# Kernel optimization log

Measured on AMD Instinct MI355X. Metric: run time of the kernel, lower is better.

The kernel has to match this reference:

```python
import jax, jax.numpy as jnp
import numpy as np

N = 50000
E = 800000
IN_C = 128
HID = 256
OUT_C = 51


def graph_conv(x, edge_index, edge_weight, w_rel, b_rel, w_root):
    # PyG GraphConv: out = lin_rel(aggr_add(w_e * x_src)) + lin_root(x)
    src, dst = edge_index[0], edge_index[1]
    msgs = x[src] * edge_weight[:, None]            # [E, F]
    agg = jax.ops.segment_sum(msgs, dst, num_segments=x.shape[0])  # [N, F]
    return agg @ w_rel + b_rel + x @ w_root


def setup_inputs() -> dict:
    key = jax.random.key(0)
    ks = jax.random.split(key, 10)
    s = lambda fan_in: 1.0 / np.sqrt(fan_in)
    return {
        "x0": jax.random.normal(ks[0], (N, IN_C), jnp.float32),
        "edge_index": jax.random.randint(ks[1], (2, E), 0, N, jnp.int64),
        "edge_weight": jax.random.uniform(ks[2], (E,), jnp.float32),
        "conv1_w_rel": jax.random.uniform(ks[3], (IN_C, HID), jnp.float32, -s(IN_C), s(IN_C)),
        "conv1_b_rel": jnp.zeros((HID,), jnp.float32),
        "conv1_w_root": jax.random.uniform(ks[4], (IN_C, HID), jnp.float32, -s(IN_C), s(IN_C)),
        "conv2_w_rel": jax.random.uniform(ks[5], (HID, HID), jnp.float32, -s(HID), s(HID)),
        "conv2_b_rel": jnp.zeros((HID,), jnp.float32),
        "conv2_w_root": jax.random.uniform(ks[6], (HID, HID), jnp.float32, -s(HID), s(HID)),
        "lin_w": jax.random.uniform(ks[7], (2 * HID, OUT_C), jnp.float32, -s(2 * HID), s(2 * HID)),
        "lin_b": jnp.zeros((OUT_C,), jnp.float32),
    }


def reference(x0, edge_index, edge_weight,
              conv1_w_rel, conv1_b_rel, conv1_w_root,
              conv2_w_rel, conv2_b_rel, conv2_w_root,
              lin_w, lin_b):
    # eval mode: dropout is identity
    x1 = jax.nn.relu(graph_conv(x0, edge_index, edge_weight, conv1_w_rel, conv1_b_rel, conv1_w_root))
    x2 = jax.nn.relu(graph_conv(x1, edge_index, edge_weight, conv2_w_rel, conv2_b_rel, conv2_w_root))
    x = jnp.concatenate([x1, x2], axis=-1)          # [N, 2H]
    return x @ lin_w + lin_b                         # [N, OUT_C]
```

## Files before the change

### kernel.cpp

```cpp
#include <hip/hip_runtime.h>
#include <hip/hip_bf16.h>

#define N_NODES 50000
#define N_EDGES 800000
#define IN_CH   128
#define HID     256
#define OUTC    51

typedef __attribute__((ext_vector_type(8))) short  bf16x8;
typedef __attribute__((ext_vector_type(4))) float  f32x4;
typedef __attribute__((ext_vector_type(2))) float  f32x2;
typedef __attribute__((ext_vector_type(4))) unsigned int u32x4;

__device__ __forceinline__ float bf2f(unsigned short u) {
    union { unsigned int i; float f; } v; v.i = ((unsigned int)u) << 16; return v.f;
}
__device__ __forceinline__ unsigned short f2bf(float f) {
    union { float f; unsigned int i; } v; v.f = f;
    unsigned int u = v.i;
    unsigned int r = (u + 0x7fffu + ((u >> 16) & 1u)) >> 16;
    return (unsigned short)r;
}
__device__ __forceinline__ unsigned short ldbf(const void* p, long i, int isf) {
    return isf ? f2bf(((const float*)p)[i]) : ((const unsigned short*)p)[i];
}
__device__ __forceinline__ float ldf(const void* p, long i, int isf) {
    return isf ? ((const float*)p)[i] : bf2f(((const unsigned short*)p)[i]);
}
__device__ __forceinline__ void load_edge_nt(const int* __restrict__ ei, int e, int is64,
                                             int* src, int* dst) {
    if (is64) { *src = __builtin_nontemporal_load(ei + 2 * e);
                *dst = __builtin_nontemporal_load(ei + 2 * (N_EDGES + e)); }
    else      { *src = __builtin_nontemporal_load(ei + e);
                *dst = __builtin_nontemporal_load(ei + N_EDGES + e); }
}

typedef const __attribute__((address_space(1))) unsigned int* gas_u32;
typedef __attribute__((address_space(3))) unsigned int* las_u32;
__device__ __forceinline__ void cp16(const void* g, void* l) {
    __builtin_amdgcn_global_load_lds((gas_u32)g, (las_u32)l, 16, 0, 0);
}

#define EBLK 1024
#define HB   ((N_EDGES + EBLK - 1) / EBLK)
#define NBKT ((N_NODES + 255) / 256)

#define NCHUNK ((N_NODES + 63) / 64)
#define ABLK   (NCHUNK * 4)

__global__ __launch_bounds__(256) void init_kernel(const unsigned int* __restrict__ x0w,
                                                   int* __restrict__ flags,
                                                   const int* __restrict__ ei) {
    int tid = threadIdx.x;
    if (blockIdx.x == 0) {
        if (tid < 64) {
            unsigned int w = x0w[tid];
            unsigned int ex = (w >> 7) & 0xFFu;
            unsigned long long bm = __ballot(ex >= 0x60u && ex <= 0x90u);
            if (tid == 0) flags[0] = (__popcll(bm) >= 48) ? 0 : 1;
        }
        return;
    }
    __shared__ int any;
    if (tid == 0) any = 0;
    __syncthreads();
    int acc = 0;
    for (int s = 0; s < 8; s++) {
        int i = (tid * 8 + s) * (N_EDGES / 2048);
        acc |= ei[2 * i + 1];
    }
    if (acc != 0) any = 1;
    __syncthreads();
    if (tid == 0) flags[1] = any;
}

__global__ void prep_all_kernel(const void* __restrict__ x0, int cb,
                                const void* __restrict__ w1r, const void* __restrict__ w1x,
                                const void* __restrict__ w2r, const void* __restrict__ w2x,
                                const void* __restrict__ lw,
                                const void* __restrict__ b1h, const void* __restrict__ b2h,
                                const void* __restrict__ lbh, const int* __restrict__ flags,
                                unsigned short* __restrict__ x0bf,
                                unsigned short* __restrict__ Bt1, unsigned short* __restrict__ Bt2,
                                unsigned short* __restrict__ Bt3,
                                float* __restrict__ b1, float* __restrict__ b2, float* __restrict__ b3,
                                const int* __restrict__ ei, unsigned int* __restrict__ bc,
                                int pblocks) {
    __shared__ unsigned int cnt[NBKT];
    int isf = flags[0];
    if ((int)blockIdx.x < cb) {
        if (!isf) return;
        long t0 = ((long)blockIdx.x * 256 + threadIdx.x) * 8;
        const float* xf = (const float*)x0;
        f32x4 v0 = *(const f32x4*)(xf + t0);
        f32x4 v1 = *(const f32x4*)(xf + t0 + 4);
        u32x4 pk;
        pk[0] = (unsigned int)f2bf(v0[0]) | ((unsigned int)f2bf(v0[1]) << 16);
        pk[1] = (unsigned int)f2bf(v0[2]) | ((unsigned int)f2bf(v0[3]) << 16);
        pk[2] = (unsigned int)f2bf(v1[0]) | ((unsigned int)f2bf(v1[1]) << 16);
        pk[3] = (unsigned int)f2bf(v1[2]) | ((unsigned int)f2bf(v1[3]) << 16);
        *(u32x4*)(x0bf + t0) = pk;
        return;
    }
    int rb = blockIdx.x - cb;
    if (rb >= pblocks) {
        int b = rb - pblocks;
        int tid = threadIdx.x;
        if (tid < NBKT) cnt[tid] = 0;
        __syncthreads();
        int is64 = (flags[1] == 0);
        int e0 = b * EBLK;
#pragma unroll
        for (int u = 0; u < 4; u++) {
            int e = e0 + u * 256 + tid;
            if (e < N_EDGES) {
                int src, dst; load_edge_nt(ei, e, is64, &src, &dst);
                if ((unsigned)src < N_NODES && (unsigned)dst < N_NODES)
                    atomicAdd(&cnt[dst >> 8], 1u);
            }
        }
        __syncthreads();
        if (tid < NBKT) bc[tid * HB + b] = cnt[tid];
        return;
    }
    int t = rb * 256 + threadIdx.x;
    if (t < 256 * 256) {
        int n = t >> 8, k = t & 255;
        Bt1[n * 256 + k] = (k < 128) ? ldbf(w1r, k * 256 + n, isf) : ldbf(w1x, (k - 128) * 256 + n, isf);
        return;
    }
    t -= 256 * 256;
    if (t < 256 * 512) {
        int n = t >> 9, k = t & 511;
        Bt2[n * 512 + k] = (k < 256) ? ldbf(w2r, k * 256 + n, isf) : ldbf(w2x, (k - 256) * 256 + n, isf);
        return;
    }
    t -= 256 * 512;
    if (t < 64 * 512) {
        int n = t >> 9, k = t & 511;
        Bt3[n * 512 + k] = (n < OUTC) ? ldbf(lw, k * OUTC + n, isf) : (unsigned short)0;
        return;
    }
    t -= 64 * 512;
    if (t < 256) { b1[t] = ldf(b1h, t, isf); return; }
    t -= 256;
    if (t < 256) { b2[t] = ldf(b2h, t, isf); return; }
    t -= 256;
    if (t < 64)  { b3[t] = (t < OUTC) ? ldf(lbh, t, isf) : 0.0f; return; }
}

__global__ __launch_bounds__(1024) void s1_kernel(const unsigned int* __restrict__ bc,
                                                  unsigned int* __restrict__ pbase,
                                                  unsigned int* __restrict__ total) {
    __shared__ unsigned int sd[1024];
    int b = blockIdx.x, tid = threadIdx.x;
    unsigned int v = (tid < HB) ? bc[b * HB + tid] : 0u;
    sd[tid] = v;
    __syncthreads();
    for (int off = 1; off < 1024; off <<= 1) {
        unsigned int t = (tid >= off) ? sd[tid - off] : 0u;
        __syncthreads();
        sd[tid] += t;
        __syncthreads();
    }
    if (tid < HB) pbase[tid * NBKT + b] = sd[tid] - v;
    if (tid == 1023) total[b] = sd[1023];
}

__global__ __launch_bounds__(256) void f1_kernel(const int* __restrict__ ei, const void* __restrict__ ew,
                                                 const int* __restrict__ flags,
                                                 const unsigned int* __restrict__ pbase,
                                                 const unsigned int* __restrict__ btot,
                                                 uint2* __restrict__ rec) {
    __shared__ unsigned int cur[NBKT];
    __shared__ unsigned int sb[256];
    int tid = threadIdx.x;
    unsigned int v = (tid < NBKT) ? btot[tid] : 0u;
    sb[tid] = v;
    __syncthreads();
    for (int off = 1; off < 256; off <<= 1) {
        unsigned int t = (tid >= off) ? sb[tid - off] : 0u;
        __syncthreads();
        sb[tid] += t;
        __syncthreads();
    }
    if (tid < NBKT) cur[tid] = (sb[tid] - v) + pbase[blockIdx.x * NBKT + tid];
    __syncthreads();
    int is64 = (flags[1] == 0);
    int isf = flags[0];
    int e0 = blockIdx.x * EBLK;
#pragma unroll
    for (int u = 0; u < 4; u++) {
        int e = e0 + u * 256 + tid;
        if (e < N_EDGES) {
            int src, dst; load_edge_nt(ei, e, is64, &src, &dst);
            if ((unsigned)src < N_NODES && (unsigned)dst < N_NODES) {
                unsigned int w = ldbf(ew, e, isf);
                unsigned int pos = atomicAdd(&cur[dst >> 8], 1u);
                uint2 r; r.x = (w << 16) | (unsigned)src; r.y = (unsigned)dst;
                rec[pos] = r;
            }
        }
    }
}

__global__ __launch_bounds__(512) void f2_kernel(const uint2* __restrict__ rec,
                                                 const unsigned int* __restrict__ btot,
                                                 int* __restrict__ rp, unsigned int* __restrict__ cw) {
    __shared__ unsigned int sb[256], c2[256], sc[256], cur2[256];
    int tid = threadIdx.x, b = blockIdx.x;
    unsigned int vb = 0;
    if (tid < 256) { vb = (tid < NBKT) ? btot[tid] : 0u; sb[tid] = vb; }
    __syncthreads();
    for (int off = 1; off < 256; off <<= 1) {
        unsigned int t = (tid < 256 && tid >= off) ? sb[tid - off] : 0u;
        __syncthreads();
        if (tid < 256) sb[tid] += t;
        __syncthreads();
    }
    unsigned int s0 = (b > 0) ? sb[b - 1] : 0u;
    unsigned int e0 = sb[b];
    if (b == 0 && tid == 0) rp[N_NODES] = (int)sb[NBKT - 1];
    if (tid < 256) c2[tid] = 0;
    __syncthreads();
    for (unsigned int pos = s0 + tid; pos < e0; pos += 512)
        atomicAdd(&c2[rec[pos].y & 255u], 1u);
    __syncthreads();
    unsigned int v = 0;
    if (tid < 256) { v = c2[tid]; sc[tid] = v; }
    __syncthreads();
    for (int off = 1; off < 256; off <<= 1) {
        unsigned int t = (tid < 256 && tid >= off) ? sc[tid - off] : 0u;
        __syncthreads();
        if (tid < 256) sc[tid] += t;
        __syncthreads();
    }
    if (tid < 256) {
        unsigned int start = s0 + sc[tid] - v;
        int node = b * 256 + tid;
        if (node < N_NODES) rp[node] = (int)start;
        cur2[tid] = start;
    }
    __syncthreads();
    for (unsigned int pos = s0 + tid; pos < e0; pos += 512) {
        uint2 r = rec[pos];
        unsigned int p = atomicAdd(&cur2[r.y & 255u], 1u);
        cw[p] = r.x;
    }
}

__global__ __launch_bounds__(256) void zout_kernel(unsigned short* __restrict__ out, long n) {
    long t = (long)blockIdx.x * 256 + threadIdx.x;
    if (t < n) out[t] = 0;
}

__global__ __launch_bounds__(256) void agg1_kernel(const unsigned short* __restrict__ x0raw,
                                                   const unsigned short* __restrict__ x0conv,
                                                   int use_conv, const int* __restrict__ flags,
                                                   const int* __restrict__ rp, const unsigned int* __restrict__ cw,
                                                   unsigned short* __restrict__ X12) {
    const unsigned short* x0b = (use_conv && flags[0]) ? x0conv : x0raw;
    int bid = blockIdx.x;
    int qq = (bid >> 1) & 3;
    int chunk = (bid >> 3) * 2 + (bid & 1);
    int g = threadIdx.x >> 4;
    int l = threadIdx.x & 15;
    int grpbase = threadIdx.x & 48;
    const unsigned short* tab = x0b + qq * 32 + l * 2;
#pragma unroll 1
    for (int i = 0; i < 4; i++) {
        int r = chunk * 64 + i * 16 + g;
        if (r >= N_NODES) continue;
        int js = rp[r], je = rp[r + 1];
        if (js < 0) js = 0;
        if (je > N_EDGES) je = N_EDGES;
        float a0 = 0.f, a1 = 0.f;
        for (int base = js; base < je; base += 16) {
            int n = je - base; if (n > 16) n = 16;
            int idx = base + l; if (idx >= je) idx = je - 1;
            unsigned int rec = __builtin_nontemporal_load(cw + idx);
            for (int j = 0; j < n; j += 8) {
                int m = n - j; if (m > 8) m = 8;
                unsigned int vv[8], qd[8];
#pragma unroll
                for (int u = 0; u < 8; u++) vv[u] = __shfl(rec, grpbase + j + u);
#pragma unroll
                for (int u = 0; u < 8; u++) if (u < m)
                    qd[u] = *(const unsigned int*)(tab + (long)(vv[u] & 0xFFFFu) * 128);
#pragma unroll
                for (int u = 0; u < 8; u++) if (u < m) {
                    float w = bf2f((unsigned short)(vv[u] >> 16));
                    a0 += w * bf2f((unsigned short)(qd[u] & 0xffffu));
                    a1 += w * bf2f((unsigned short)(qd[u] >> 16));
                }
            }
        }
        *(unsigned int*)&X12[(long)r * 512 + 256 + qq * 32 + l * 2] =
            (unsigned int)f2bf(a0) | ((unsigned int)f2bf(a1) << 16);
    }
}

__global__ __launch_bounds__(256) void agg2_kernel(const int* __restrict__ rp, const unsigned int* __restrict__ cw,
                                                   unsigned short* __restrict__ X12,
                                                   const unsigned char* __restrict__ x1f8,
                                                   const int* __restrict__ flags, int f8mode) {
    int usef8 = (f8mode == 2) || (f8mode == 1 && flags[0] == 0);
    int bid = blockIdx.x;
    int qq = (bid >> 1) & 3;
    int chunk = (bid >> 3) * 2 + (bid & 1);
    int g = threadIdx.x >> 4;
    int l = threadIdx.x & 15;
    int grpbase = threadIdx.x & 48;
#pragma unroll 1
    for (int i = 0; i < 4; i++) {
        int r = chunk * 64 + i * 16 + g;
        if (r >= N_NODES) continue;
        int js = rp[r], je = rp[r + 1];
        if (js < 0) js = 0;
        if (je > N_EDGES) je = N_EDGES;
        float a0 = 0.f, a1 = 0.f, a2 = 0.f, a3 = 0.f;
        if (usef8) {
            const unsigned char* tab = x1f8 + qq * 64 + l * 4;
            for (int base = js; base < je; base += 16) {
                int n = je - base; if (n > 16) n = 16;
                int idx = base + l; if (idx >= je) idx = je - 1;
                unsigned int rec = __builtin_nontemporal_load(cw + idx);
                for (int j = 0; j < n; j += 8) {
                    int m = n - j; if (m > 8) m = 8;
                    unsigned int vv[8], qd[8];
#pragma unroll
                    for (int u = 0; u < 8; u++) vv[u] = __shfl(rec, grpbase + j + u);
#pragma unroll
                    for (int u = 0; u < 8; u++) if (u < m)
                        qd[u] = *(const unsigned int*)(tab + (long)(vv[u] & 0xFFFFu) * 256);
#pragma unroll
                    for (int u = 0; u < 8; u++) if (u < m) {
                        float w = bf2f((unsigned short)(vv[u] >> 16));
                        f32x2 plo = __builtin_amdgcn_cvt_pk_f32_fp8((int)qd[u], false);
                        f32x2 phi = __builtin_amdgcn_cvt_pk_f32_fp8((int)qd[u], true);
                        a0 += w * plo.x; a1 += w * plo.y;
                        a2 += w * phi.x; a3 += w * phi.y;
                    }
                }
            }
        } else {
            const unsigned short* tabb = X12 + qq * 64 + l * 4;
            for (int base = js; base < je; base += 16) {
                int n = je - base; if (n > 16) n = 16;
                int idx = base + l; if (idx >= je) idx = je - 1;
                unsigned int rec = __builtin_nontemporal_load(cw + idx);
                for (int j = 0; j < n; j += 8) {
                    int m = n - j; if (m > 8) m = 8;
                    unsigned int vv[8]; uint2 qd[8];
#pragma unroll
                    for (int u = 0; u < 8; u++) vv[u] = __shfl(rec, grpbase + j + u);
#pragma unroll
                    for (int u = 0; u < 8; u++) if (u < m)
                        qd[u] = *(const uint2*)(tabb + (long)(vv[u] & 0xFFFFu) * 512);
#pragma unroll
                    for (int u = 0; u < 8; u++) if (u < m) {
                        float w = bf2f((unsigned short)(vv[u] >> 16));
                        a0 += w * bf2f((unsigned short)(qd[u].x & 0xffffu));
                        a1 += w * bf2f((unsigned short)(qd[u].x >> 16));
                        a2 += w * bf2f((unsigned short)(qd[u].y & 0xffffu));
                        a3 += w * bf2f((unsigned short)(qd[u].y >> 16));
                    }
                }
            }
        }
        uint2 pk;
        pk.x = (unsigned int)f2bf(a0) | ((unsigned int)f2bf(a1) << 16);
        pk.y = (unsigned int)f2bf(a2) | ((unsigned int)f2bf(a3) << 16);
        *(uint2*)&X12[(long)r * 512 + 256 + qq * 64 + l * 4] = pk;
    }
}

__global__ __launch_bounds__(512) void gemm_big_kernel(
    const unsigned short* __restrict__ Aagg, int lda_agg, int Kagg,
    const unsigned short* __restrict__ AxRaw, const unsigned short* __restrict__ AxConv,
    int use_conv, int lda_x,
    const unsigned short* __restrict__ Bt, int K,
    const float* __restrict__ bias, const int* __restrict__ flags,
    unsigned short* __restrict__ out, int ldo, int ocol, int M,
    unsigned char* __restrict__ x1f8, int f8mode) {
    __shared__ __align__(16) unsigned short As[128][64];
    __shared__ __align__(16) unsigned short Bs[256][64];
    const unsigned short* Ax = (use_conv && flags[0]) ? AxConv : AxRaw;
    int dof8 = (f8mode == 2) || (f8mode == 1 && flags[0] == 0);
    int tid = threadIdx.x;
    int bm0 = blockIdx.x * 128;
    int wave = tid >> 6, lane = tid & 63;
    int wm = wave >> 2, wn = wave & 3;
    int quad = lane >> 4, l16 = lane & 15;
    int lr = lane >> 3;
    int sc = (lane & 7) ^ lr;

    f32x4 acc[4][4];
#pragma unroll
    for (int mt = 0; mt < 4; mt++)
#pragma unroll
        for (int nt = 0; nt < 4; nt++) acc[mt][nt] = (f32x4){0.f, 0.f, 0.f, 0.f};

    for (int k0 = 0; k0 < K; k0 += 64) {
        const unsigned short* srcp;
        int stride, koff;
        if (k0 < Kagg) { srcp = Aagg; stride = lda_agg; koff = k0; }
        else           { srcp = Ax;   stride = lda_x;   koff = k0 - Kagg; }
#pragma unroll
        for (int i = 0; i < 2; i++) {
            int t = wave * 2 + i;
            int r = t * 8 + lr;
            int gr = bm0 + r; if (gr >= M) gr = M - 1;
            cp16(srcp + (long)gr * stride + koff + sc * 8, (char*)As + t * 1024);
        }
#pragma unroll
        for (int i = 0; i < 4; i++) {
            int t = wave * 4 + i;
            int r = t * 8 + lr;
            cp16(Bt + (long)r * K + k0 + sc * 8, (char*)Bs + t * 1024);
        }
        __syncthreads();
#pragma unroll
        for (int kc = 0; kc < 64; kc += 32) {
            int k8 = (kc >> 3) + quad;
            int swz = (k8 ^ (l16 & 7)) << 4;
            bf16x8 a[4], b[4];
#pragma unroll
            for (int mt = 0; mt < 4; mt++) {
                int row = wm * 64 + mt * 16 + l16;
                a[mt] = *(const bf16x8*)((const char*)As + row * 128 + swz);
            }
#pragma unroll
            for (int nt = 0; nt < 4; nt++) {
                int row = wn * 64 + nt * 16 + l16;
                b[nt] = *(const bf16x8*)((const char*)Bs + row * 128 + swz);
            }
#pragma unroll
            for (int mt = 0; mt < 4; mt++)
#pragma unroll
                for (int nt = 0; nt < 4; nt++)
                    acc[mt][nt] = __builtin_amdgcn_mfma_f32_16x16x32_bf16(a[mt], b[nt], acc[mt][nt], 0, 0, 0);
        }
        __syncthreads();
    }

#pragma unroll
    for (int mt = 0; mt < 4; mt++) {
#pragma unroll
        for (int nt = 0; nt < 4; nt++) {
            f32x4 a = acc[mt][nt];
            int colI = wn * 64 + nt * 16 + l16;
            float bv = bias[colI];
#pragma unroll
            for (int rr = 0; rr < 4; rr++) {
                int row = bm0 + wm * 64 + mt * 16 + quad * 4 + rr;
                if (row < M) {
                    float v = a[rr] + bv;
                    v = v > 0.f ? v : 0.f;
                    out[(long)row * ldo + ocol + colI] = f2bf(v);
                    if (dof8) {
                        int p = __builtin_amdgcn_cvt_pk_fp8_f32(v, v, 0, false);
                        x1f8[(long)row * 256 + colI] = (unsigned char)(p & 0xff);
                    }
                }
            }
        }
    }
}

__global__ __launch_bounds__(256) void gemm_head_kernel(
    const unsigned short* __restrict__ Ax, int lda_x,
    const unsigned short* __restrict__ Bt, int K,
    const float* __restrict__ bias,
    void* __restrict__ out, int ldo,
    int M, int realN, const int* __restrict__ flagF) {
    __shared__ __align__(16) unsigned short As[64][64];
    __shared__ __align__(16) unsigned short Bs[64][64];
    int tid = threadIdx.x;
    int bm0 = blockIdx.x * 64;
    int wave = tid >> 6, lane = tid & 63;
    int wm = wave >> 1, wn = wave & 1;
    int quad = lane >> 4, l16 = lane & 15;
    int lr = lane >> 3;
    int sc = (lane & 7) ^ lr;

    f32x4 acc[2][2];
#pragma unroll
    for (int mt = 0; mt < 2; mt++)
#pragma unroll
        for (int nt = 0; nt < 2; nt++) acc[mt][nt] = (f32x4){0.f, 0.f, 0.f, 0.f};

    for (int k0 = 0; k0 < K; k0 += 64) {
#pragma unroll
        for (int i = 0; i < 2; i++) {
            int t = wave * 2 + i;
            int r = t * 8 + lr;
            int gr = bm0 + r; if (gr >= M) gr = M - 1;
            cp16(Ax + (long)gr * lda_x + k0 + sc * 8, (char*)As + t * 1024);
        }
#pragma unroll
        for (int i = 0; i < 2; i++) {
            int t = wave * 2 + i;
            int r = t * 8 + lr;
            cp16(Bt + (long)r * K + k0 + sc * 8, (char*)Bs + t * 1024);
        }
        __syncthreads();
#pragma unroll
        for (int kc = 0; kc < 64; kc += 32) {
            int k8 = (kc >> 3) + quad;
            int swz = (k8 ^ (l16 & 7)) << 4;
            bf16x8 a0 = *(const bf16x8*)((const char*)As + (wm * 32 + l16) * 128 + swz);
            bf16x8 a1 = *(const bf16x8*)((const char*)As + (wm * 32 + 16 + l16) * 128 + swz);
#pragma unroll
            for (int nt = 0; nt < 2; nt++) {
                bf16x8 b = *(const bf16x8*)((const char*)Bs + (wn * 32 + nt * 16 + l16) * 128 + swz);
                acc[0][nt] = __builtin_amdgcn_mfma_f32_16x16x32_bf16(a0, b, acc[0][nt], 0, 0, 0);
                acc[1][nt] = __builtin_amdgcn_mfma_f32_16x16x32_bf16(a1, b, acc[1][nt], 0, 0, 0);
            }
        }
        __syncthreads();
    }

    int out_f32 = *flagF;
#pragma unroll
    for (int mt = 0; mt < 2; mt++) {
#pragma unroll
        for (int nt = 0; nt < 2; nt++) {
            f32x4 a = acc[mt][nt];
            int colI = wn * 32 + nt * 16 + l16;
            float bv = bias[colI];
#pragma unroll
            for (int rr = 0; rr < 4; rr++) {
                int row = bm0 + wm * 32 + mt * 16 + quad * 4 + rr;
                if (row < M && colI < realN) {
                    float v = a[rr] + bv;
                    long idx = (long)row * ldo + colI;
                    if (out_f32) ((float*)out)[idx] = v;
                    else ((unsigned short*)out)[idx] = f2bf(v);
                }
            }
        }
    }
}

extern "C" void kernel_launch(void* const* d_in, const int* in_sizes, int n_in,
                              void* d_out, int out_size, void* d_ws, size_t ws_size,
                              hipStream_t stream) {
    const void* x0  = d_in[0];
    const int*  ei  = (const int*)d_in[1];
    const void* ew  = d_in[2];
    const void* w1r = d_in[3];
    const void* b1h = d_in[4];
    const void* w1x = d_in[5];
    const void* w2r = d_in[6];
    const void* b2h = d_in[7];
    const void* w2x = d_in[8];
    const void* lw  = d_in[9];
    const void* lbh = d_in[10];

    char* ws = (char*)d_ws;
    unsigned short* X12     = (unsigned short*)(ws);
    unsigned int*   cw      = (unsigned int*)(ws + 51200000);
    int*            row_ptr = (int*)(ws + 54400000);
    unsigned short* Bt1     = (unsigned short*)(ws + 54800128);
    unsigned short* Bt2     = (unsigned short*)(ws + 54931200);
    unsigned short* Bt3     = (unsigned short*)(ws + 55193344);
    float*          b1      = (float*)(ws + 55258880);
    float*          b2      = (float*)(ws + 55259904);
    float*          b3      = (float*)(ws + 55260928);
    int*            flags   = (int*)(ws + 55261184);
    unsigned short* x0bf    = (unsigned short*)(ws + 55262272);
    unsigned char*  x1f8sep = (unsigned char*)(ws + 68062272);
    const size_t NEED_NOCONV = 55262272;
    const size_t NEED_FULL   = 68062272;
    const size_t NEED_F8SEP  = 80862272;

    uint2*        rec   = (uint2*)(ws);
    unsigned int* bc    = (unsigned int*)(ws + 6400000);
    unsigned int* pbse  = (unsigned int*)(ws + 7013120);
    unsigned int* btot  = (unsigned int*)(ws + 7626240);

    if (ws_size < NEED_NOCONV) {
        long n = (long)N_NODES * OUTC;
        zout_kernel<<<(int)((n + 255) / 256), 256, 0, stream>>>((unsigned short*)d_out, n);
        return;
    }
    int use_conv = (ws_size >= NEED_FULL) ? 1 : 0;
    int f8mode = (ws_size >= NEED_F8SEP) ? 2 : (use_conv ? 1 : 0);
    unsigned char* x1f8 = (f8mode == 2) ? x1f8sep : (unsigned char*)x0bf;

    int* flagF = flags + 0;

    init_kernel<<<2, 256, 0, stream>>>((const unsigned int*)x0, flags, ei);

    int cb = use_conv ? ((N_NODES * IN_CH) / (256 * 8)) : 0;
    {
        int ptotal = 256 * 256 + 256 * 512 + 64 * 512 + 256 + 256 + 64;
        int pblocks = (ptotal + 255) / 256;
        prep_all_kernel<<<cb + pblocks + HB, 256, 0, stream>>>(
            x0, cb, w1r, w1x, w2r, w2x, lw, b1h, b2h, lbh, flags, x0bf,
            Bt1, Bt2, Bt3, b1, b2, b3, ei, bc, pblocks);
    }

    s1_kernel<<<NBKT, 1024, 0, stream>>>(bc, pbse, btot);
    f1_kernel<<<HB, 256, 0, stream>>>(ei, ew, flags, pbse, btot, rec);
    f2_kernel<<<NBKT, 512, 0, stream>>>(rec, btot, row_ptr, cw);

    int mblocks  = (N_NODES + 127) / 128;
    int hblocks  = (N_NODES + 63) / 64;

    const unsigned short* x0raw = (const unsigned short*)x0;

    agg1_kernel<<<ABLK, 256, 0, stream>>>(x0raw, x0bf, use_conv, flags, row_ptr, cw, X12);
    gemm_big_kernel<<<mblocks, 512, 0, stream>>>(X12 + 256, 512, 128,
                                                 x0raw, x0bf, use_conv, IN_CH,
                                                 Bt1, 256, b1, flags,
                                                 X12, 512, 0, N_NODES, x1f8, f8mode);
    agg2_kernel<<<ABLK, 256, 0, stream>>>(row_ptr, cw, X12, x1f8, flags, f8mode);
    gemm_big_kernel<<<mblocks, 512, 0, stream>>>(X12 + 256, 512, 256,
                                                 X12, X12, 0, 512,
                                                 Bt2, 512, b2, flags,
                                                 X12, 512, 256, N_NODES, (unsigned char*)nullptr, 0);
    gemm_head_kernel<<<hblocks, 256, 0, stream>>>(X12, 512, Bt3, 512, b3,
                                                  d_out, OUTC, N_NODES, OUTC, flagF);
}
```

Measured before the change: 294.9 us.

## Gather full rows in agg1 and split fp8 x1 table into column quarters

agg1 now assigns one 16-lane group per destination row and gathers each source's full 128-feature row with 16-byte loads, replacing four passes over the edge list with 4-byte loads. The fp8 copy of x1 is stored as four 64-column planes (QSZ apart), so each agg2 quarter gathers from a compact 3.2 MB table that is more likely to stay cache-resident. Trade-offs are higher register use for eight accumulators in agg1 and an fp8 buffer layout that must hold 4*QSZ bytes.

```diff
diff --git a/kernel.cpp b/kernel.cpp
--- a/kernel.cpp
+++ b/kernel.cpp
@@ -6,6 +6,8 @@
 #define IN_CH   128
 #define HID     256
 #define OUTC    51
+
+#define QSZ 3200000
 
 typedef __attribute__((ext_vector_type(8))) short  bf16x8;
 typedef __attribute__((ext_vector_type(4))) float  f32x4;
@@ -46,7 +48,7 @@
 #define NBKT ((N_NODES + 255) / 256)
 
 #define NCHUNK ((N_NODES + 63) / 64)
-#define ABLK   (NCHUNK * 4)
+#define ABLKQ  (NCHUNK * 4)
 
 __global__ __launch_bounds__(256) void init_kernel(const unsigned int* __restrict__ x0w,
                                                    int* __restrict__ flags,
@@ -260,57 +262,62 @@
                                                    const int* __restrict__ rp, const unsigned int* __restrict__ cw,
                                                    unsigned short* __restrict__ X12) {
     const unsigned short* x0b = (use_conv && flags[0]) ? x0conv : x0raw;
+    int r = blockIdx.x * 16 + (threadIdx.x >> 4);
+    if (r >= N_NODES) return;
+    int l = threadIdx.x & 15;
+    int grpbase = threadIdx.x & 48;
+    int js = rp[r], je = rp[r + 1];
+    if (js < 0) js = 0;
+    if (je > N_EDGES) je = N_EDGES;
+    float a0 = 0.f, a1 = 0.f, a2 = 0.f, a3 = 0.f;
+    float a4 = 0.f, a5 = 0.f, a6 = 0.f, a7 = 0.f;
+    for (int base = js; base < je; base += 16) {
+        int n = je - base; if (n > 16) n = 16;
+        int idx = base + l; if (idx >= je) idx = je - 1;
+        unsigned int rec = __builtin_nontemporal_load(cw + idx);
+        for (int j = 0; j < n; j += 4) {
+            int m = n - j; if (m > 4) m = 4;
+            unsigned int vv[4]; u32x4 q[4];
+#pragma unroll
+            for (int u = 0; u < 4; u++) vv[u] = __shfl(rec, grpbase + j + u);
+#pragma unroll
+            for (int u = 0; u < 4; u++) if (u < m)
+                q[u] = *(const u32x4*)(x0b + (long)(vv[u] & 0xFFFFu) * 128 + l * 8);
+#pragma unroll
+            for (int u = 0; u < 4; u++) if (u < m) {
+                float w = bf2f((unsigned short)(vv[u] >> 16));
+                a0 += w * bf2f((unsigned short)(q[u][0] & 0xffffu));
+                a1 += w * bf2f((unsigned short)(q[u][0] >> 16));
+                a2 += w * bf2f((unsigned short)(q[u][1] & 0xffffu));
+                a3 += w * bf2f((unsigned short)(q[u][1] >> 16));
+                a4 += w * bf2f((unsigned short)(q[u][2] & 0xffffu));
+                a5 += w * bf2f((unsigned short)(q[u][2] >> 16));
+                a6 += w * bf2f((unsigned short)(q[u][3] & 0xffffu));
+                a7 += w * bf2f((unsigned short)(q[u][3] >> 16));
+            }
+        }
+    }
+    u32x4 pk;
+    pk[0] = (unsigned int)f2bf(a0) | ((unsigned int)f2bf(a1) << 16);
+    pk[1] = (unsigned int)f2bf(a2) | ((unsigned int)f2bf(a3) << 16);
+    pk[2] = (unsigned int)f2bf(a4) | ((unsigned int)f2bf(a5) << 16);
+    pk[3] = (unsigned int)f2bf(a6) | ((unsigned int)f2bf(a7) << 16);
+    *(u32x4*)&X12[(long)r * 512 + 256 + l * 8] = pk;
+}
+
+__global__ __launch_bounds__(256) void agg2_kernel(const int* __restrict__ rp, const unsigned int* __restrict__ cw,
+                                                   unsigned short* __restrict__ X12,
+                                                   const unsigned char* __restrict__ x1f8q,
+                                                   const int* __restrict__ flags, int f8mode) {
+    int usef8 = (f8mode == 2) || (f8mode == 1 && flags[0] == 0);
     int bid = blockIdx.x;
-    int qq = (bid >> 1) & 3;
-    int chunk = (bid >> 3) * 2 + (bid & 1);
+    int qq = bid & 3;
+    int chunk = bid >> 2;
     int g = threadIdx.x >> 4;
     int l = threadIdx.x & 15;
     int grpbase = threadIdx.x & 48;
-    const unsigned short* tab = x0b + qq * 32 + l * 2;
-#pragma unroll 1
-    for (int i = 0; i < 4; i++) {
-        int r = chunk * 64 + i * 16 + g;
-        if (r >= N_NODES) continue;
-        int js = rp[r], je = rp[r + 1];
-        if (js < 0) js = 0;
-        if (je > N_EDGES) je = N_EDGES;
-        float a0 = 0.f, a1 = 0.f;
-        for (int base = js; base < je; base += 16) {
-            int n = je - base; if (n > 16) n = 16;
-            int idx = base + l; if (idx >= je) idx = je - 1;
-            unsigned int rec = __builtin_nontemporal_load(cw + idx);
-            for (int j = 0; j < n; j += 8) {
-                int m = n - j; if (m > 8) m = 8;
-                unsigned int vv[8], qd[8];
-#pragma unroll
-                for (int u = 0; u < 8; u++) vv[u] = __shfl(rec, grpbase + j + u);
-#pragma unroll
-                for (int u = 0; u < 8; u++) if (u < m)
-                    qd[u] = *(const unsigned int*)(tab + (long)(vv[u] & 0xFFFFu) * 128);
-#pragma unroll
-                for (int u = 0; u < 8; u++) if (u < m) {
-                    float w = bf2f((unsigned short)(vv[u] >> 16));
-                    a0 += w * bf2f((unsigned short)(qd[u] & 0xffffu));
-                    a1 += w * bf2f((unsigned short)(qd[u] >> 16));
-                }
-            }
-        }
-        *(unsigned int*)&X12[(long)r * 512 + 256 + qq * 32 + l * 2] =
-            (unsigned int)f2bf(a0) | ((unsigned int)f2bf(a1) << 16);
-    }
-}
-
-__global__ __launch_bounds__(256) void agg2_kernel(const int* __restrict__ rp, const unsigned int* __restrict__ cw,
-                                                   unsigned short* __restrict__ X12,
-                                                   const unsigned char* __restrict__ x1f8,
-                                                   const int* __restrict__ flags, int f8mode) {
-    int usef8 = (f8mode == 2) || (f8mode == 1 && flags[0] == 0);
-    int bid = blockIdx.x;
-    int qq = (bid >> 1) & 3;
-    int chunk = (bid >> 3) * 2 + (bid & 1);
-    int g = threadIdx.x >> 4;
-    int l = threadIdx.x & 15;
-    int grpbase = threadIdx.x & 48;
+    const unsigned char* tab = x1f8q + (long)qq * QSZ + l * 4;
+    const unsigned short* tabb = X12 + qq * 64 + l * 4;
 #pragma unroll 1
     for (int i = 0; i < 4; i++) {
         int r = chunk * 64 + i * 16 + g;
@@ -320,7 +327,6 @@
         if (je > N_EDGES) je = N_EDGES;
         float a0 = 0.f, a1 = 0.f, a2 = 0.f, a3 = 0.f;
         if (usef8) {
-            const unsigned char* tab = x1f8 + qq * 64 + l * 4;
             for (int base = js; base < je; base += 16) {
                 int n = je - base; if (n > 16) n = 16;
                 int idx = base + l; if (idx >= je) idx = je - 1;
@@ -332,7 +338,7 @@
                     for (int u = 0; u < 8; u++) vv[u] = __shfl(rec, grpbase + j + u);
 #pragma unroll
                     for (int u = 0; u < 8; u++) if (u < m)
-                        qd[u] = *(const unsigned int*)(tab + (long)(vv[u] & 0xFFFFu) * 256);
+                        qd[u] = *(const unsigned int*)(tab + (long)(vv[u] & 0xFFFFu) * 64);
 #pragma unroll
                     for (int u = 0; u < 8; u++) if (u < m) {
                         float w = bf2f((unsigned short)(vv[u] >> 16));
@@ -344,7 +350,6 @@
                 }
             }
         } else {
-            const unsigned short* tabb = X12 + qq * 64 + l * 4;
             for (int base = js; base < je; base += 16) {
                 int n = je - base; if (n > 16) n = 16;
                 int idx = base + l; if (idx >= je) idx = je - 1;
@@ -382,7 +387,7 @@
     const unsigned short* __restrict__ Bt, int K,
     const float* __restrict__ bias, const int* __restrict__ flags,
     unsigned short* __restrict__ out, int ldo, int ocol, int M,
-    unsigned char* __restrict__ x1f8, int f8mode) {
+    unsigned char* __restrict__ x1f8q, int f8mode) {
     __shared__ __align__(16) unsigned short As[128][64];
     __shared__ __align__(16) unsigned short Bs[256][64];
     const unsigned short* Ax = (use_conv && flags[0]) ? AxConv : AxRaw;
@@ -460,7 +465,8 @@
                     out[(long)row * ldo + ocol + colI] = f2bf(v);
                     if (dof8) {
                         int p = __builtin_amdgcn_cvt_pk_fp8_f32(v, v, 0, false);
-                        x1f8[(long)row * 256 + colI] = (unsigned char)(p & 0xff);
+                        x1f8q[(long)(colI >> 6) * QSZ + (long)row * 64 + (colI & 63)] =
+                            (unsigned char)(p & 0xff);
                     }
                 }
             }
@@ -608,19 +614,21 @@
 
     int mblocks  = (N_NODES + 127) / 128;
     int hblocks  = (N_NODES + 63) / 64;
+    int ablocks  = (N_NODES + 15) / 16;
 
     const unsigned short* x0raw = (const unsigned short*)x0;
 
-    agg1_kernel<<<ABLK, 256, 0, stream>>>(x0raw, x0bf, use_conv, flags, row_ptr, cw, X12);
+    agg1_kernel<<<ablocks, 256, 0, stream>>>(x0raw, x0bf, use_conv, flags, row_ptr, cw, X12);
     gemm_big_kernel<<<mblocks, 512, 0, stream>>>(X12 + 256, 512, 128,
                                                  x0raw, x0bf, use_conv, IN_CH,
                                                  Bt1, 256, b1, flags,
                                                  X12, 512, 0, N_NODES, x1f8, f8mode);
-    agg2_kernel<<<ABLK, 256, 0, stream>>>(row_ptr, cw, X12, x1f8, flags, f8mode);
+    agg2_kernel<<<ABLKQ, 256, 0, stream>>>(row_ptr, cw, X12, x1f8, flags, f8mode);
     gemm_big_kernel<<<mblocks, 512, 0, stream>>>(X12 + 256, 512, 256,
                                                  X12, X12, 0, 512,
                                                  Bt2, 512, b2, flags,
-                                                 X12, 512, 256, N_NODES, (unsigned char*)nullptr, 0);
+                                                 X12, 512, 256, N_NODES,
+                                                 (unsigned char*)nullptr, 0);
     gemm_head_kernel<<<hblocks, 256, 0, stream>>>(X12, 512, Bt3, 512, b3,
                                                   d_out, OUTC, N_NODES, OUTC, flagF);
 }
```

After: 278.9 us. 1.06x faster.
